# Performance work log

Measured on AMD Instinct MI355X. Metric: run time of the kernel, lower is better.

Reference implementation:

```python
import jax, jax.numpy as jnp
import numpy as np

DIM, HEADS, WS = 256, 16, 8
B, H, W = 2, 252, 252
BN_EPS = 1e-5


def _rel_index():
    # Same construction as the torch buffer relative_position_index (64,64)
    coords = np.stack(np.meshgrid(np.arange(WS), np.arange(WS), indexing='ij'))
    flat = coords.reshape(2, -1)
    rel = (flat[:, :, None] - flat[:, None, :]).transpose(1, 2, 0).copy()
    rel[..., 0] += WS - 1
    rel[..., 1] += WS - 1
    rel[..., 0] *= 2 * WS - 1
    return jnp.asarray(rel.sum(-1))

REL_IDX = _rel_index()  # (WS*WS, WS*WS) int


def _conv(x, w, pad, groups=1):
    return jax.lax.conv_general_dilated(
        x, w, (1, 1), [(pad[0], pad[0]), (pad[1], pad[1])],
        dimension_numbers=('NCHW', 'OIHW', 'NCHW'), feature_group_count=groups)


def setup_inputs() -> dict:
    key = jax.random.key(0)
    ks = jax.random.split(key, 8)
    s = lambda k, shape, sc: jax.random.normal(k, shape, jnp.float32) * sc
    z = lambda: jnp.zeros((DIM,), jnp.float32)
    return {
        'x': s(ks[0], (B, DIM, H, W), 1.0),
        'w_qkv': s(ks[1], (3 * DIM, DIM, 1, 1), 0.05),
        'rel_bias_table': s(ks[2], ((2 * WS - 1) ** 2, HEADS), 0.02),
        'w_h': s(ks[3], (DIM, DIM, WS, 1), 0.02),
        'b_h': z(),
        'w_v': s(ks[4], (DIM, DIM, 1, WS), 0.02),
        'b_v': z(),
        'w_dw': s(ks[5], (DIM, 1, WS, WS), 0.05),
        'bn_gamma': jnp.ones((DIM,), jnp.float32),
        'bn_beta': z(),
        'bn_mean': z(),
        'bn_var': jnp.ones((DIM,), jnp.float32),
        'w_pw': s(ks[6], (DIM, DIM, 1, 1), 0.05),
    }


def reference(x, w_qkv, rel_bias_table, w_h, b_h, w_v, b_v, w_dw,
              bn_gamma, bn_beta, bn_mean, bn_var, w_pw):
    Bc, C, Hc, Wc = x.shape
    pad_h, pad_w = WS - Hc % WS, WS - Wc % WS
    xp = jnp.pad(x, ((0, 0), (0, 0), (0, pad_h), (0, pad_w)), mode='reflect')
    Hp, Wp = Hc + pad_h, Wc + pad_w
    hh, ww, d = Hp // WS, Wp // WS, C // HEADS

    qkv = _conv(xp, w_qkv, (0, 0))  # (B, 3C, Hp, Wp)
    # b (qkv h d) (hh ws1) (ww ws2) -> qkv (b hh ww) h (ws1 ws2) d
    qkv = qkv.reshape(Bc, 3, HEADS, d, hh, WS, ww, WS)
    qkv = qkv.transpose(1, 0, 4, 6, 2, 5, 7, 3).reshape(3, Bc * hh * ww, HEADS, WS * WS, d)
    q, k, v = qkv[0], qkv[1], qkv[2]

    dots = jnp.einsum('nhid,nhjd->nhij', q, k) * (d ** -0.5)
    bias = rel_bias_table[REL_IDX.reshape(-1)].reshape(WS * WS, WS * WS, HEADS)
    dots = dots + bias.transpose(2, 0, 1)[None]  # (1, h, 64, 64)
    attn = jax.nn.softmax(dots, axis=-1)
    out = jnp.einsum('nhij,nhjd->nhid', attn, v)
    # (b hh ww) h (ws1 ws2) d -> b (h d) (hh ws1) (ww ws2)
    out = out.reshape(Bc, hh, ww, HEADS, WS, WS, d)
    out = out.transpose(0, 3, 6, 1, 4, 2, 5).reshape(Bc, C, Hp, Wp)
    out = out[:, :, :Hc, :Wc]

    p1 = _conv(jnp.pad(out, ((0, 0), (0, 0), (0, 1), (0, 0)), mode='reflect'),
               w_h, (WS // 2 - 1, 0)) + b_h[None, :, None, None]
    p2 = _conv(jnp.pad(out, ((0, 0), (0, 0), (0, 0), (0, 1)), mode='reflect'),
               w_v, (0, WS // 2 - 1)) + b_v[None, :, None, None]
    y = jnp.pad(p1 + p2, ((0, 0), (0, 0), (0, 1), (0, 1)), mode='reflect')
    y = _conv(y, w_dw, ((WS - 1) // 2, (WS - 1) // 2), groups=DIM)  # depthwise
    inv = bn_gamma / jnp.sqrt(bn_var + BN_EPS)
    y = y * inv[None, :, None, None] + (bn_beta - bn_mean * inv)[None, :, None, None]
    y = _conv(y, w_pw, (0, 0))  # pointwise 1x1
    return y[:, :, :Hc, :Wc]
```

## Files before the change

kernel.cpp:

```cpp
#include <hip/hip_runtime.h>
#include <hip/hip_bf16.h>

#define HC 252
#define WC 252
#define CD 256
#define NHEADS 16

#define XP_W 264
#define XP_HW (252*264)
#define XP_CHW (256*252*264)

typedef unsigned short u16;
typedef unsigned int u32;
typedef __attribute__((ext_vector_type(8))) short bf16x8;
typedef __attribute__((ext_vector_type(4))) float f32x4;
typedef __attribute__((ext_vector_type(4))) u32 u32x4;
typedef __attribute__((ext_vector_type(2))) u32 u32x2;

#define XP_BYTES (2u * (unsigned)XP_CHW * 2u)
#define ZP_OFF   XP_BYTES
#define ZP_BYTES 409600u
#define WT_OFF   (ZP_OFF + ZP_BYTES)
#define WT_ELEMS (128*8192)
#define WPW_OFF  (WT_OFF + (unsigned)WT_ELEMS*2u)
#define WPW_ELEMS (8*8192)
#define WQ_OFF   (WPW_OFF + (unsigned)WPW_ELEMS*2u)
#define WQ_ELEMS (768*256)
#define BIAS_OFF (WQ_OFF + (unsigned)WQ_ELEMS*2u)

__device__ __forceinline__ u16 bfu(float f) {
    __hip_bfloat16 h = __float2bfloat16(f);
    return *(reinterpret_cast<u16*>(&h));
}
__device__ __forceinline__ u32 pack2(float a, float b) {
    return (u32)bfu(a) | ((u32)bfu(b) << 16);
}
__device__ __forceinline__ float bf2f(u16 v) {
    union { u32 u; float f; } cv; cv.u = ((u32)v) << 16; return cv.f;
}

__global__ __launch_bounds__(256, 2) void attn_mfma(
    const float* __restrict__ x, const u16* __restrict__ WQ,
    const float* __restrict__ BIASF, u16* __restrict__ xp)
{
    __shared__ __align__(16) char smem[73728];

    const int bid = blockIdx.x;
    const int zz = (bid & 7) * 256 + (bid >> 3);
    const int wx = zz & 31, wy = (zz >> 5) & 31, b = zz >> 10;
    const int tid = threadIdx.x;
    const int lane = tid & 63, wid = tid >> 6;
    const int g = lane >> 4, li = lane & 15;

    {
        int ci = tid;
        const float* srcc = x + (size_t)(b * 256 + ci) * (HC * WC);
        #pragma unroll
        for (int r = 0; r < 8; ++r) {
            int h = wy * 8 + r; if (h >= HC) h = 2 * HC - 2 - h;
            const float* src = srcc + h * WC;
            float v[8];
            if (wx == 31) {
                #pragma unroll
                for (int c = 0; c < 8; ++c) {
                    int w = 248 + c; if (w >= WC) w = 2 * WC - 2 - w;
                    v[c] = src[w];
                }
            } else {
                float4 f0 = *(const float4*)(src + wx * 8);
                float4 f1 = *(const float4*)(src + wx * 8 + 4);
                v[0]=f0.x; v[1]=f0.y; v[2]=f0.z; v[3]=f0.w;
                v[4]=f1.x; v[5]=f1.y; v[6]=f1.z; v[7]=f1.w;
            }
            #pragma unroll
            for (int c = 0; c < 8; ++c) {
                int pos = r * 8 + c;
                int byte = pos * 512 + ((ci * 2) ^ ((pos & 7) << 4));
                *(u16*)(smem + byte) = bfu(v[c]);
            }
        }
    }
    __syncthreads();

    const int WB = 32768 + wid * 10240;
    char* Qb = smem + WB;
    char* Kb = smem + WB + 2048;
    char* Vb = smem + WB + 4096;
    char* Pb = smem + WB + 6144;

    const bf16x8 zf = {0,0,0,0,0,0,0,0};

    #pragma unroll 1
    for (int hh = 0; hh < 4; ++hh) {
        const int head = wid * 4 + hh;

        f32x4 acc[3][4];
        #pragma unroll
        for (int p = 0; p < 3; ++p)
            #pragma unroll
            for (int nf = 0; nf < 4; ++nf) acc[p][nf] = (f32x4){0.f,0.f,0.f,0.f};

        for (int ks = 0; ks < 8; ++ks) {
            bf16x8 bx[4];
            #pragma unroll
            for (int nf = 0; nf < 4; ++nf) {
                int pos = 16 * nf + li;
                int byte = pos * 512 + ((ks * 64 + 16 * g) ^ ((pos & 7) << 4));
                bx[nf] = *(const bf16x8*)(smem + byte);
            }
            bf16x8 aw[3];
            #pragma unroll
            for (int p = 0; p < 3; ++p) {
                int o = p * 256 + head * 16 + li;
                aw[p] = *(const bf16x8*)(WQ + o * 256 + ks * 32 + 8 * g);
            }
            __builtin_amdgcn_s_setprio(1);
            #pragma unroll
            for (int p = 0; p < 3; ++p)
                #pragma unroll
                for (int nf = 0; nf < 4; ++nf)
                    acc[p][nf] = __builtin_amdgcn_mfma_f32_16x16x32_bf16(aw[p], bx[nf], acc[p][nf], 0, 0, 0);
            __builtin_amdgcn_s_setprio(0);
        }

        #pragma unroll
        for (int p = 0; p < 3; ++p) {
            if (p < 2) {
                char* base = (p == 0) ? Qb : Kb;
                #pragma unroll
                for (int nf = 0; nf < 4; ++nf) {
                    int pos = 16 * nf + li;
                    u32 lo = pack2(acc[p][nf][0], acc[p][nf][1]);
                    u32 hi = pack2(acc[p][nf][2], acc[p][nf][3]);
                    int byte = pos * 32 + ((8 * g) ^ (((pos >> 2) & 1) << 4));
                    *(u32x2*)(base + byte) = (u32x2){lo, hi};
                }
            } else {
                #pragma unroll
                for (int nf = 0; nf < 4; ++nf) {
                    int pos = 16 * nf + li;
                    #pragma unroll
                    for (int r = 0; r < 4; ++r) {
                        int d = 4 * g + r;
                        int byte = (pos >> 3) * 256 + d * 16 + (pos & 7) * 2;
                        *(u16*)(Vb + byte) = bfu(acc[p][nf][r]);
                    }
                }
            }
        }

        f32x4 s[4][4];
        #pragma unroll
        for (int mf = 0; mf < 4; ++mf)
            #pragma unroll
            for (int nf = 0; nf < 4; ++nf) s[mf][nf] = (f32x4){0.f,0.f,0.f,0.f};
        bf16x8 bk[4];
        #pragma unroll
        for (int nf = 0; nf < 4; ++nf) {
            int pos = 16 * nf + li;
            bk[nf] = (g < 2) ? *(const bf16x8*)(Kb + pos * 32 + ((16 * g) ^ (((pos >> 2) & 1) << 4))) : zf;
        }
        __builtin_amdgcn_s_setprio(1);
        #pragma unroll
        for (int mf = 0; mf < 4; ++mf) {
            int pos = 16 * mf + li;
            bf16x8 aq = (g < 2) ? *(const bf16x8*)(Qb + pos * 32 + ((16 * g) ^ (((pos >> 2) & 1) << 4))) : zf;
            #pragma unroll
            for (int nf = 0; nf < 4; ++nf)
                s[mf][nf] = __builtin_amdgcn_mfma_f32_16x16x32_bf16(aq, bk[nf], s[mf][nf], 0, 0, 0);
        }
        __builtin_amdgcn_s_setprio(0);

        f32x4 e[4][4];
        f32x4 rs[4];
        #pragma unroll
        for (int mf = 0; mf < 4; ++mf) rs[mf] = (f32x4){0.f,0.f,0.f,0.f};
        #pragma unroll
        for (int mf = 0; mf < 4; ++mf)
            #pragma unroll
            for (int nf = 0; nf < 4; ++nf) {
                f32x4 b4 = *(const f32x4*)(BIASF + (((head * 4 + mf) * 4 + nf) * 64 + lane) * 4);
                #pragma unroll
                for (int r = 0; r < 4; ++r) {
                    float ev = __expf(s[mf][nf][r] * 0.25f + b4[r]);
                    e[mf][nf][r] = ev;
                    rs[mf][r] += ev;
                }
            }
        #pragma unroll
        for (int mf = 0; mf < 4; ++mf)
            #pragma unroll
            for (int r = 0; r < 4; ++r) {
                float t = rs[mf][r];
                t += __shfl_xor(t, 1); t += __shfl_xor(t, 2);
                t += __shfl_xor(t, 4); t += __shfl_xor(t, 8);
                rs[mf][r] = t;
            }

        f32x4 o[4];
        #pragma unroll
        for (int mf = 0; mf < 4; ++mf) o[mf] = (f32x4){0.f,0.f,0.f,0.f};
        const bool even = !(lane & 1);
        #pragma unroll
        for (int hf = 0; hf < 2; ++hf) {
            #pragma unroll
            for (int mf = 0; mf < 4; ++mf)
                #pragma unroll
                for (int nfl = 0; nfl < 2; ++nfl) {
                    f32x4 ee = e[mf][2 * hf + nfl];
                    float p0 = __shfl_xor(ee[0], 1), p1 = __shfl_xor(ee[1], 1);
                    float p2 = __shfl_xor(ee[2], 1), p3 = __shfl_xor(ee[3], 1);
                    int jl = 16 * nfl + (li & ~1);
                    u32 w0, w1; int r0;
                    if (even) { w0 = pack2(ee[0], p0); w1 = pack2(ee[1], p1); r0 = 0; }
                    else      { w0 = pack2(p2, ee[2]); w1 = pack2(p3, ee[3]); r0 = 2; }
                    int i0 = 16 * mf + 4 * g + r0, i1 = i0 + 1;
                    *(u32*)(Pb + i0 * 64 + ((2 * jl) ^ ((i0 & 3) << 4))) = w0;
                    *(u32*)(Pb + i1 * 64 + ((2 * jl) ^ ((i1 & 3) << 4))) = w1;
                }
            bf16x8 bv = *(const bf16x8*)(Vb + (4 * hf + g) * 256 + li * 16);
            __builtin_amdgcn_s_setprio(1);
            #pragma unroll
            for (int mf = 0; mf < 4; ++mf) {
                int i = 16 * mf + li;
                bf16x8 ap = *(const bf16x8*)(Pb + i * 64 + ((16 * g) ^ ((i & 3) << 4)));
                o[mf] = __builtin_amdgcn_mfma_f32_16x16x32_bf16(ap, bv, o[mf], 0, 0, 0);
            }
            __builtin_amdgcn_s_setprio(0);
        }

        #pragma unroll
        for (int mf = 0; mf < 4; ++mf) {
            int h = wy * 8 + 2 * mf + (g >> 1);
            int wbase = wx * 8 + 4 * (g & 1);
            if (h < HC && wbase < WC) {
                float v0 = o[mf][0] / rs[mf][0], v1 = o[mf][1] / rs[mf][1];
                float v2 = o[mf][2] / rs[mf][2], v3 = o[mf][3] / rs[mf][3];
                size_t idx = ((size_t)(b * 256 + head * 16 + li) * HC + h) * XP_W + wbase + 4;
                *(u32x2*)(xp + idx) = (u32x2){pack2(v0, v1), pack2(v2, v3)};
            }
        }
    }
}

__global__ __launch_bounds__(256) void wprep_kernel(
    const float* __restrict__ wh, const float* __restrict__ wv,
    const float* __restrict__ wpw, const float* __restrict__ wqkv,
    const float* __restrict__ btab, u16* __restrict__ wsu)
{
    int i = blockIdx.x * 256 + threadIdx.x;
    u16* WT = wsu + WT_OFF / 2;
    u16* WP = wsu + WPW_OFF / 2;
    u16* ZP = wsu + ZP_OFF / 2;
    u16* WQp = wsu + WQ_OFF / 2;
    float* BF = (float*)(wsu + BIAS_OFF / 2);
    if (i < WT_ELEMS) {
        int j = i & 7, l = (i >> 3) & 1023, s = i >> 13;
        int kb = (l >> 8) & 3;
        int co = (l & 255) ^ (kb << 1);
        float v = (s < 64) ? wh[co * 2048 + s * 32 + kb * 8 + j]
                           : wv[co * 2048 + (s - 64) * 32 + kb * 8 + j];
        WT[i] = bfu(v);
    } else if (i < WT_ELEMS + WPW_ELEMS) {
        int i2 = i - WT_ELEMS;
        int j = i2 & 7, l = (i2 >> 3) & 1023, s = i2 >> 13;
        int kb = (l >> 8) & 3;
        int co = (l & 255) ^ (kb << 1);
        WP[i2] = bfu(wpw[co * 256 + s * 32 + kb * 8 + j]);
    } else if (i < WT_ELEMS + WPW_ELEMS + (int)(ZP_BYTES / 2)) {
        ZP[i - WT_ELEMS - WPW_ELEMS] = 0;
    } else if (i < WT_ELEMS + WPW_ELEMS + (int)(ZP_BYTES / 2) + WQ_ELEMS) {
        int i4 = i - WT_ELEMS - WPW_ELEMS - (int)(ZP_BYTES / 2);
        WQp[i4] = bfu(wqkv[i4]);
    } else {
        int i5 = i - WT_ELEMS - WPW_ELEMS - (int)(ZP_BYTES / 2) - WQ_ELEMS;
        if (i5 < 16384) {
            int lane = i5 & 63, nf = (i5 >> 6) & 3, mf = (i5 >> 8) & 3, head = i5 >> 10;
            int gg = lane >> 4, ll = lane & 15;
            #pragma unroll
            for (int r = 0; r < 4; ++r) {
                int row = 16 * mf + 4 * gg + r;
                int col = 16 * nf + ll;
                int dy = (row >> 3) - (col >> 3) + 7;
                int dx = (row & 7) - (col & 7) + 7;
                BF[i5 * 4 + r] = btab[(dy * 15 + dx) * NHEADS + head];
            }
        }
    }
}

__global__ __launch_bounds__(256) void halo_kernel(u16* __restrict__ xp)
{
    int i = blockIdx.x * 256 + threadIdx.x;
    if (i >= 129024 * 12) return;
    int row = i / 12, c = i % 12;
    int wp = (c < 4) ? c : 252 + c;
    u16 v = 0;
    if (wp == 256) v = xp[row * XP_W + 254];
    xp[row * XP_W + wp] = v;
}

__global__ __launch_bounds__(512, 2) void sepconv_mfma(
    const u16* __restrict__ xp, const u16* __restrict__ WT,
    const u16* __restrict__ ZP,
    const float* __restrict__ b_h, const float* __restrict__ b_v,
    u16* __restrict__ P)
{
    __shared__ __align__(16) u16 As[2][8192];
    __shared__ __align__(16) u16 Bs[2][256 * 36];

    const int bid = blockIdx.x;
    const int zz = (bid & 7) * 63 + (bid >> 3);
    const int h = zz % HC, b = zz / HC;
    const int tid = threadIdx.x;
    const int lane = tid & 63, wid = tid >> 6;
    const int wr = wid >> 2, wc = wid & 3;
    const int cq = lane & 15, kb = lane >> 4;

    const int wl2 = (tid & 127) * 2;
    const int oc = tid >> 7;

    const u16* hcur[8];
    int hstep[8];
    #pragma unroll
    for (int t = 0; t < 8; ++t) {
        int j = h + t - 3;
        bool valid = (j >= 0 && j <= 252);
        int jr = (j == 252) ? 250 : j;
        hcur[t] = valid ? (xp + (size_t)b * XP_CHW + (size_t)jr * XP_W) : ZP;
        hstep[t] = valid ? 4 * XP_HW : 0;
    }
    const u16* vbase = xp + (size_t)b * XP_CHW + (size_t)h * XP_W;
    const int hvoff = oc * XP_HW + wl2 + 4;

    const int bw0 = wl2 * 36 + oc * 8;
    const int bw1 = bw0 + 36;

    f32x4 acc[8][4];
    #pragma unroll
    for (int m = 0; m < 8; ++m)
        #pragma unroll
        for (int n = 0; n < 4; ++n) acc[m][n] = (f32x4){0.f, 0.f, 0.f, 0.f};

    u32x4 rA[2];
    u32 rB[8];

    rA[0] = *(const u32x4*)(WT + (size_t)tid * 8);
    rA[1] = *(const u32x4*)(WT + (size_t)(512 + tid) * 8);
    #pragma unroll
    for (int t = 0; t < 8; ++t)
        rB[t] = *(const u32*)(hcur[t] + hvoff);
    *(u32x4*)&As[0][(size_t)tid * 8] = rA[0];
    *(u32x4*)&As[0][(size_t)(512 + tid) * 8] = rA[1];
    {
        union { bf16x8 v; u32 u[4]; } p0, p1;
        #pragma unroll
        for (int q = 0; q < 4; ++q) {
            p0.u[q] = __builtin_amdgcn_perm(rB[2 * q + 1], rB[2 * q], 0x05040100u);
            p1.u[q] = __builtin_amdgcn_perm(rB[2 * q + 1], rB[2 * q], 0x07060302u);
        }
        *(bf16x8*)&Bs[0][bw0] = p0.v;
        *(bf16x8*)&Bs[0][bw1] = p1.v;
    }

    #pragma unroll 1
    for (int s = 0; s < 128; ++s) {
        const int cur = s & 1;
        const int s1 = s + 1;
        const bool hph1 = (s1 < 64);
        if (s1 < 128) {
            rA[0] = *(const u32x4*)(WT + (size_t)s1 * 8192 + (size_t)tid * 8);
            rA[1] = *(const u32x4*)(WT + (size_t)s1 * 8192 + (size_t)(512 + tid) * 8);
            if (hph1) {
                #pragma unroll
                for (int t = 0; t < 8; ++t) hcur[t] += hstep[t];
                #pragma unroll
                for (int t = 0; t < 8; ++t)
                    rB[t] = *(const u32*)(hcur[t] + hvoff);
            } else {
                int off = ((s1 - 64) * 4 + oc) * XP_HW + wl2;
                #pragma unroll
                for (int l = 0; l < 6; ++l)
                    rB[l] = *(const u32*)(vbase + off + 2 * l);
            }
        }
        __syncthreads();

        {
            bf16x8 af[8], bfr[4];
            #pragma unroll
            for (int m = 0; m < 8; ++m) {
                int row = wr * 128 + m * 16 + cq;
                af[m] = *(const bf16x8*)&As[cur][(kb * 256 + (row ^ (kb << 1))) * 8];
            }
            #pragma unroll
            for (int n = 0; n < 4; ++n)
                bfr[n] = *(const bf16x8*)&Bs[cur][(wc * 64 + n * 16 + cq) * 36 + kb * 8];
            __builtin_amdgcn_s_setprio(1);
            #pragma unroll
            for (int m = 0; m < 8; ++m)
                #pragma unroll
                for (int n = 0; n < 4; ++n)
                    acc[m][n] = __builtin_amdgcn_mfma_f32_16x16x32_bf16(af[m], bfr[n], acc[m][n], 0, 0, 0);
            __builtin_amdgcn_s_setprio(0);
        }

        if (s1 < 128) {
            const int nxt = cur ^ 1;
            *(u32x4*)&As[nxt][(size_t)tid * 8] = rA[0];
            *(u32x4*)&As[nxt][(size_t)(512 + tid) * 8] = rA[1];
            union { bf16x8 v; u32 u[4]; } p0, p1;
            if (hph1) {
                #pragma unroll
                for (int q = 0; q < 4; ++q) {
                    p0.u[q] = __builtin_amdgcn_perm(rB[2 * q + 1], rB[2 * q], 0x05040100u);
                    p1.u[q] = __builtin_amdgcn_perm(rB[2 * q + 1], rB[2 * q], 0x07060302u);
                }
            } else {
                #pragma unroll
                for (int q = 0; q < 4; ++q)
                    p0.u[q] = __builtin_amdgcn_alignbit(rB[q + 1], rB[q], 16);
                p1.u[0] = rB[1]; p1.u[1] = rB[2];
                p1.u[2] = rB[3]; p1.u[3] = rB[4];
            }
            *(bf16x8*)&Bs[nxt][bw0] = p0.v;
            *(bf16x8*)&Bs[nxt][bw1] = p1.v;
        }
    }

    const int rq = lane >> 4, cc = lane & 15;
    #pragma unroll
    for (int m = 0; m < 8; ++m) {
        int cgb = wr * 128 + m * 16 + rq * 4;
        float bias[4];
        #pragma unroll
        for (int rr = 0; rr < 4; ++rr) bias[rr] = b_h[cgb + rr] + b_v[cgb + rr];
        #pragma unroll
        for (int n = 0; n < 4; ++n) {
            int wg = wc * 64 + n * 16 + cc;
            if (wg < WC) {
                #pragma unroll
                for (int rr = 0; rr < 4; ++rr)
                    P[((size_t)(b * CD + cgb + rr) * HC + h) * WC + wg] = bfu(acc[m][n][rr] + bias[rr]);
            }
        }
    }
}

__global__ __launch_bounds__(256) void dwbn_kernel(
    const u16* __restrict__ P, const float* __restrict__ w_dw,
    const float* __restrict__ gamma, const float* __restrict__ beta,
    const float* __restrict__ mean, const float* __restrict__ var,
    __hip_bfloat16* __restrict__ Yb)
{
    __shared__ float ps[15][42];
    __shared__ float wd[64];
    const int bw = blockIdx.x, bh = blockIdx.y, bz = blockIdx.z;
    const int b = bz >> 8, c = bz & 255;
    const int h0 = bh * 8, w0 = bw * 32;
    const int tid = threadIdx.x;
    if (tid < 64) wd[tid] = w_dw[c * 64 + tid];
    for (int it = 0; it < 3; ++it) {
        int flat = tid + it * 256;
        if (flat < 630) {
            int row = flat / 42, col = flat % 42;
            int j = h0 - 3 + row, wcol = w0 - 3 + col;
            float v = 0.f;
            if (j >= 0 && j <= HC && wcol >= 0 && wcol <= WC) {
                int jr = (j == HC) ? (HC - 2) : j;
                int wr2 = (wcol == WC) ? (WC - 2) : wcol;
                v = bf2f(P[((size_t)(b * CD + c) * HC + jr) * WC + wr2]);
            }
            ps[row][col] = v;
        }
    }
    __syncthreads();
    const int r = tid >> 5, cc = tid & 31;
    const int h = h0 + r, w = w0 + cc;
    if (h < HC && w < WC) {
        float s = 0.f;
        #pragma unroll
        for (int u = 0; u < 8; ++u)
            #pragma unroll
            for (int v2 = 0; v2 < 8; ++v2)
                s += wd[u * 8 + v2] * ps[r + u][cc + v2];
        const float inv = gamma[c] * rsqrtf(var[c] + 1e-5f);
        Yb[((b * CD + c) * HC + h) * WC + w] = __float2bfloat16(s * inv + (beta[c] - mean[c] * inv));
    }
}

__global__ __launch_bounds__(512, 2) void pw_mfma(
    const u16* __restrict__ Y, const u16* __restrict__ WP,
    float* __restrict__ O)
{
    __shared__ __align__(16) u16 As[2][8192];
    __shared__ __align__(16) u16 Bs[2][256 * 36];

    const int bid = blockIdx.x;
    const int zz = (bid & 7) * 63 + (bid >> 3);
    const int h = zz % HC, b = zz / HC;
    const int tid = threadIdx.x;
    const int lane = tid & 63, wid = tid >> 6;
    const int wr = wid >> 2, wc = wid & 3;
    const int cq = lane & 15, kb = lane >> 4;

    const int wl2 = (tid & 127) * 2;
    const int oc = tid >> 7;

    const u16* yb = Y + ((size_t)(b * 256 + oc * 8) * HC + h) * WC + wl2;

    const int bw0 = wl2 * 36 + oc * 8;
    const int bw1 = bw0 + 36;

    f32x4 acc[8][4];
    #pragma unroll
    for (int m = 0; m < 8; ++m)
        #pragma unroll
        for (int n = 0; n < 4; ++n) acc[m][n] = (f32x4){0.f, 0.f, 0.f, 0.f};

    u32x4 rA[2];
    u32 rB[8];

    rA[0] = *(const u32x4*)(WP + (size_t)tid * 8);
    rA[1] = *(const u32x4*)(WP + (size_t)(512 + tid) * 8);
    #pragma unroll
    for (int j = 0; j < 8; ++j)
        rB[j] = *(const u32*)(yb + (size_t)j * (HC * WC));
    *(u32x4*)&As[0][(size_t)tid * 8] = rA[0];
    *(u32x4*)&As[0][(size_t)(512 + tid) * 8] = rA[1];
    {
        union { bf16x8 v; u32 u[4]; } p0, p1;
        #pragma unroll
        for (int q = 0; q < 4; ++q) {
            p0.u[q] = __builtin_amdgcn_perm(rB[2 * q + 1], rB[2 * q], 0x05040100u);
            p1.u[q] = __builtin_amdgcn_perm(rB[2 * q + 1], rB[2 * q], 0x07060302u);
        }
        *(bf16x8*)&Bs[0][bw0] = p0.v;
        *(bf16x8*)&Bs[0][bw1] = p1.v;
    }

    #pragma unroll 1
    for (int s = 0; s < 8; ++s) {
        const int cur = s & 1;
        const int s1 = s + 1;
        if (s1 < 8) {
            rA[0] = *(const u32x4*)(WP + (size_t)s1 * 8192 + (size_t)tid * 8);
            rA[1] = *(const u32x4*)(WP + (size_t)s1 * 8192 + (size_t)(512 + tid) * 8);
            #pragma unroll
            for (int j = 0; j < 8; ++j)
                rB[j] = *(const u32*)(yb + (size_t)(s1 * 32 + j) * (HC * WC));
        }
        __syncthreads();

        {
            bf16x8 af[8], bfr[4];
            #pragma unroll
            for (int m = 0; m < 8; ++m) {
                int row = wr * 128 + m * 16 + cq;
                af[m] = *(const bf16x8*)&As[cur][(kb * 256 + (row ^ (kb << 1))) * 8];
            }
            #pragma unroll
            for (int n = 0; n < 4; ++n)
                bfr[n] = *(const bf16x8*)&Bs[cur][(wc * 64 + n * 16 + cq) * 36 + kb * 8];
            __builtin_amdgcn_s_setprio(1);
            #pragma unroll
            for (int m = 0; m < 8; ++m)
                #pragma unroll
                for (int n = 0; n < 4; ++n)
                    acc[m][n] = __builtin_amdgcn_mfma_f32_16x16x32_bf16(af[m], bfr[n], acc[m][n], 0, 0, 0);
            __builtin_amdgcn_s_setprio(0);
        }

        if (s1 < 8) {
            const int nxt = cur ^ 1;
            *(u32x4*)&As[nxt][(size_t)tid * 8] = rA[0];
            *(u32x4*)&As[nxt][(size_t)(512 + tid) * 8] = rA[1];
            union { bf16x8 v; u32 u[4]; } p0, p1;
            #pragma unroll
            for (int q = 0; q < 4; ++q) {
                p0.u[q] = __builtin_amdgcn_perm(rB[2 * q + 1], rB[2 * q], 0x05040100u);
                p1.u[q] = __builtin_amdgcn_perm(rB[2 * q + 1], rB[2 * q], 0x07060302u);
            }
            *(bf16x8*)&Bs[nxt][bw0] = p0.v;
            *(bf16x8*)&Bs[nxt][bw1] = p1.v;
        }
    }

    const int rq = lane >> 4, cc = lane & 15;
    #pragma unroll
    for (int m = 0; m < 8; ++m) {
        int cgb = wr * 128 + m * 16 + rq * 4;
        #pragma unroll
        for (int n = 0; n < 4; ++n) {
            int wg = wc * 64 + n * 16 + cc;
            if (wg < WC) {
                #pragma unroll
                for (int rr = 0; rr < 4; ++rr)
                    O[((size_t)(b * CD + cgb + rr) * HC + h) * WC + wg] = acc[m][n][rr];
            }
        }
    }
}

extern "C" void kernel_launch(void* const* d_in, const int* in_sizes, int n_in,
                              void* d_out, int out_size, void* d_ws, size_t ws_size,
                              hipStream_t stream)
{
    const float* x      = (const float*)d_in[0];
    const float* w_qkv  = (const float*)d_in[1];
    const float* bias_t = (const float*)d_in[2];
    const float* w_h    = (const float*)d_in[3];
    const float* b_h    = (const float*)d_in[4];
    const float* w_v    = (const float*)d_in[5];
    const float* b_v    = (const float*)d_in[6];
    const float* w_dw   = (const float*)d_in[7];
    const float* bn_g   = (const float*)d_in[8];
    const float* bn_b   = (const float*)d_in[9];
    const float* bn_m   = (const float*)d_in[10];
    const float* bn_v   = (const float*)d_in[11];
    const float* w_pw   = (const float*)d_in[12];
    float* out = (float*)d_out;

    u16* wsu = (u16*)d_ws;
    const u16* XPu = wsu;
    const u16* ZPu = wsu + ZP_OFF / 2;
    const u16* WTu = wsu + WT_OFF / 2;
    const u16* WPu = wsu + WPW_OFF / 2;
    const u16* WQu = wsu + WQ_OFF / 2;
    const float* BFu = (const float*)(wsu + BIAS_OFF / 2);

    wprep_kernel<<<5984, 256, 0, stream>>>(w_h, w_v, w_pw, w_qkv, bias_t, wsu);
    attn_mfma<<<2048, 256, 0, stream>>>(x, WQu, BFu, wsu);
    halo_kernel<<<6048, 256, 0, stream>>>(wsu);
    sepconv_mfma<<<504, 512, 0, stream>>>(XPu, WTu, ZPu, b_h, b_v, (u16*)d_out);
    dwbn_kernel<<<dim3(8, 32, 512), 256, 0, stream>>>((const u16*)d_out, w_dw, bn_g, bn_b,
                                                      bn_m, bn_v, (__hip_bfloat16*)d_ws);
    pw_mfma<<<504, 512, 0, stream>>>(wsu, WPu, out);
}
```

Before: 678.1 us.

## Store attention output channel-innermost so sepconv B tiles load as contiguous vectors

The padded attention output buffer moves from (b, c, h, w) to (b, h, w, c), with channels innermost. The attention epilogue, the halo fill and the weight-prep K ordering all change to match. The separable-conv kernel can now load each B slice as two contiguous 16-byte vectors per thread and write them straight to LDS, with no byte permutes or align shifts. The cost is scattered 2-byte stores in the attention epilogue (stride 256 elements) in place of the old packed 8-byte stores.

```diff
diff --git a/kernel.cpp b/kernel.cpp
--- a/kernel.cpp
+++ b/kernel.cpp
@@ -7,8 +7,8 @@
 #define NHEADS 16
 
 #define XP_W 264
-#define XP_HW (252*264)
-#define XP_CHW (256*252*264)
+#define XP_ROW (XP_W*256)
+#define XP_BH  (252*XP_ROW)
 
 typedef unsigned short u16;
 typedef unsigned int u32;
@@ -17,7 +17,7 @@
 typedef __attribute__((ext_vector_type(4))) u32 u32x4;
 typedef __attribute__((ext_vector_type(2))) u32 u32x2;
 
-#define XP_BYTES (2u * (unsigned)XP_CHW * 2u)
+#define XP_BYTES (2u * 2u * (unsigned)XP_BH)
 #define ZP_OFF   XP_BYTES
 #define ZP_BYTES 409600u
 #define WT_OFF   (ZP_OFF + ZP_BYTES)
@@ -234,10 +234,12 @@
             int h = wy * 8 + 2 * mf + (g >> 1);
             int wbase = wx * 8 + 4 * (g & 1);
             if (h < HC && wbase < WC) {
-                float v0 = o[mf][0] / rs[mf][0], v1 = o[mf][1] / rs[mf][1];
-                float v2 = o[mf][2] / rs[mf][2], v3 = o[mf][3] / rs[mf][3];
-                size_t idx = ((size_t)(b * 256 + head * 16 + li) * HC + h) * XP_W + wbase + 4;
-                *(u32x2*)(xp + idx) = (u32x2){pack2(v0, v1), pack2(v2, v3)};
+                size_t rowb = ((size_t)(b * HC + h)) * XP_ROW + (size_t)(head * 16 + li);
+                #pragma unroll
+                for (int r = 0; r < 4; ++r) {
+                    float v = o[mf][r] / rs[mf][r];
+                    xp[rowb + (size_t)(wbase + r + 4) * 256] = bfu(v);
+                }
             }
         }
     }
@@ -258,8 +260,15 @@
         int j = i & 7, l = (i >> 3) & 1023, s = i >> 13;
         int kb = (l >> 8) & 3;
         int co = (l & 255) ^ (kb << 1);
-        float v = (s < 64) ? wh[co * 2048 + s * 32 + kb * 8 + j]
-                           : wv[co * 2048 + (s - 64) * 32 + kb * 8 + j];
+        float v;
+        if (s < 64) {
+            int t = s >> 3, ci = (s & 7) * 32 + kb * 8 + j;
+            v = wh[co * 2048 + ci * 8 + t];
+        } else {
+            int s2 = s - 64;
+            int t = s2 >> 3, ci = (s2 & 7) * 32 + kb * 8 + j;
+            v = wv[co * 2048 + ci * 8 + t];
+        }
         WT[i] = bfu(v);
     } else if (i < WT_ELEMS + WPW_ELEMS) {
         int i2 = i - WT_ELEMS;
@@ -292,16 +301,18 @@
 __global__ __launch_bounds__(256) void halo_kernel(u16* __restrict__ xp)
 {
     int i = blockIdx.x * 256 + threadIdx.x;
-    if (i >= 129024 * 12) return;
-    int row = i / 12, c = i % 12;
-    int wp = (c < 4) ? c : 252 + c;
+    if (i >= 2 * 252 * 12 * 256) return;
+    int ci = i & 255;
+    int c12 = (i >> 8) % 12;
+    int row = i / (12 * 256);
+    int wp = (c12 < 4) ? c12 : 252 + c12;
     u16 v = 0;
-    if (wp == 256) v = xp[row * XP_W + 254];
-    xp[row * XP_W + wp] = v;
+    if (wp == 256) v = xp[(size_t)row * XP_ROW + 254 * 256 + ci];
+    xp[(size_t)row * XP_ROW + (size_t)wp * 256 + ci] = v;
 }
 
 __global__ __launch_bounds__(512, 2) void sepconv_mfma(
-    const u16* __restrict__ xp, const u16* __restrict__ WT,
+    const u16* __restrict__ xpt, const u16* __restrict__ WT,
     const u16* __restrict__ ZP,
     const float* __restrict__ b_h, const float* __restrict__ b_v,
     u16* __restrict__ P)
@@ -317,24 +328,12 @@
     const int wr = wid >> 2, wc = wid & 3;
     const int cq = lane & 15, kb = lane >> 4;
 
-    const int wl2 = (tid & 127) * 2;
-    const int oc = tid >> 7;
-
-    const u16* hcur[8];
-    int hstep[8];
-    #pragma unroll
-    for (int t = 0; t < 8; ++t) {
-        int j = h + t - 3;
-        bool valid = (j >= 0 && j <= 252);
-        int jr = (j == 252) ? 250 : j;
-        hcur[t] = valid ? (xp + (size_t)b * XP_CHW + (size_t)jr * XP_W) : ZP;
-        hstep[t] = valid ? 4 * XP_HW : 0;
-    }
-    const u16* vbase = xp + (size_t)b * XP_CHW + (size_t)h * XP_W;
-    const int hvoff = oc * XP_HW + wl2 + 4;
-
-    const int bw0 = wl2 * 36 + oc * 8;
-    const int bw1 = bw0 + 36;
+    const int wB = tid & 255;
+    const int oc0 = tid >> 8;
+    const int tb = (wB + 4) * 256 + oc0 * 8;
+    const int bsw = wB * 36 + oc0 * 8;
+
+    const u16* const xb = xpt + (size_t)(b * HC) * XP_ROW;
 
     f32x4 acc[8][4];
     #pragma unroll
@@ -343,46 +342,45 @@
         for (int n = 0; n < 4; ++n) acc[m][n] = (f32x4){0.f, 0.f, 0.f, 0.f};
 
     u32x4 rA[2];
-    u32 rB[8];
+    u32x4 rB0, rB1;
+
+#define SC_SRC(t, RP, SO)                                                      \
+    if ((t) < 64) {                                                            \
+        int tt = (t) >> 3;                                                     \
+        int jt = h + tt - 3;                                                   \
+        int jr = (jt == 252) ? 250 : jt;                                       \
+        RP = (jt >= 0 && jt <= 252) ? (xpt + ((size_t)(b * HC) + jr) * XP_ROW) : ZP; \
+        SO = ((t) & 7) * 32;                                                   \
+    } else {                                                                   \
+        int tt = ((t) - 64) >> 3;                                              \
+        RP = xb + (size_t)h * XP_ROW + (tt - 3) * 256;                         \
+        SO = (((t) - 64) & 7) * 32;                                            \
+    }
 
     rA[0] = *(const u32x4*)(WT + (size_t)tid * 8);
     rA[1] = *(const u32x4*)(WT + (size_t)(512 + tid) * 8);
-    #pragma unroll
-    for (int t = 0; t < 8; ++t)
-        rB[t] = *(const u32*)(hcur[t] + hvoff);
+    {
+        const u16* rp; int so;
+        SC_SRC(0, rp, so)
+        rB0 = *(const u32x4*)(rp + so + tb);
+        rB1 = *(const u32x4*)(rp + so + tb + 16);
+    }
     *(u32x4*)&As[0][(size_t)tid * 8] = rA[0];
     *(u32x4*)&As[0][(size_t)(512 + tid) * 8] = rA[1];
-    {
-        union { bf16x8 v; u32 u[4]; } p0, p1;
-        #pragma unroll
-        for (int q = 0; q < 4; ++q) {
-            p0.u[q] = __builtin_amdgcn_perm(rB[2 * q + 1], rB[2 * q], 0x05040100u);
-            p1.u[q] = __builtin_amdgcn_perm(rB[2 * q + 1], rB[2 * q], 0x07060302u);
-        }
-        *(bf16x8*)&Bs[0][bw0] = p0.v;
-        *(bf16x8*)&Bs[0][bw1] = p1.v;
-    }
+    *(u32x4*)&Bs[0][bsw] = rB0;
+    *(u32x4*)&Bs[0][bsw + 16] = rB1;
 
     #pragma unroll 1
     for (int s = 0; s < 128; ++s) {
         const int cur = s & 1;
         const int s1 = s + 1;
-        const bool hph1 = (s1 < 64);
         if (s1 < 128) {
             rA[0] = *(const u32x4*)(WT + (size_t)s1 * 8192 + (size_t)tid * 8);
             rA[1] = *(const u32x4*)(WT + (size_t)s1 * 8192 + (size_t)(512 + tid) * 8);
-            if (hph1) {
-                #pragma unroll
-                for (int t = 0; t < 8; ++t) hcur[t] += hstep[t];
-                #pragma unroll
-                for (int t = 0; t < 8; ++t)
-                    rB[t] = *(const u32*)(hcur[t] + hvoff);
-            } else {
-                int off = ((s1 - 64) * 4 + oc) * XP_HW + wl2;
-                #pragma unroll
-                for (int l = 0; l < 6; ++l)
-                    rB[l] = *(const u32*)(vbase + off + 2 * l);
-            }
+            const u16* rp; int so;
+            SC_SRC(s1, rp, so)
+            rB0 = *(const u32x4*)(rp + so + tb);
+            rB1 = *(const u32x4*)(rp + so + tb + 16);
         }
         __syncthreads();
 
@@ -409,24 +407,11 @@
             const int nxt = cur ^ 1;
             *(u32x4*)&As[nxt][(size_t)tid * 8] = rA[0];
             *(u32x4*)&As[nxt][(size_t)(512 + tid) * 8] = rA[1];
-            union { bf16x8 v; u32 u[4]; } p0, p1;
-            if (hph1) {
-                #pragma unroll
-                for (int q = 0; q < 4; ++q) {
-                    p0.u[q] = __builtin_amdgcn_perm(rB[2 * q + 1], rB[2 * q], 0x05040100u);
-                    p1.u[q] = __builtin_amdgcn_perm(rB[2 * q + 1], rB[2 * q], 0x07060302u);
-                }
-            } else {
-                #pragma unroll
-                for (int q = 0; q < 4; ++q)
-                    p0.u[q] = __builtin_amdgcn_alignbit(rB[q + 1], rB[q], 16);
-                p1.u[0] = rB[1]; p1.u[1] = rB[2];
-                p1.u[2] = rB[3]; p1.u[3] = rB[4];
-            }
-            *(bf16x8*)&Bs[nxt][bw0] = p0.v;
-            *(bf16x8*)&Bs[nxt][bw1] = p1.v;
-        }
-    }
+            *(u32x4*)&Bs[nxt][bsw] = rB0;
+            *(u32x4*)&Bs[nxt][bsw + 16] = rB1;
+        }
+    }
+#undef SC_SRC
 
     const int rq = lane >> 4, cc = lane & 15;
     #pragma unroll
```

New measurement: 689.6 us. No clear change (+1.7%).
